# Kernel tuning notes

Hardware: AMD Instinct MI355X
Metric: run time of the kernel (lower is better)

Reference implementation:

```python
import jax, jax.numpy as jnp
import numpy as np

H = 64
IN = 3
OUT = 4


def _lstm_layer(x, w_ih, w_hh, b_ih, b_hh):
    # x: [B, T, D_in]; w_ih: [4H, D_in]; w_hh: [4H, H]; PyTorch gate order i,f,g,o
    B = x.shape[0]
    gx = jnp.einsum('btd,gd->btg', x, w_ih) + b_ih + b_hh  # [B, T, 4H]
    gx_t = jnp.swapaxes(gx, 0, 1)  # [T, B, 4H]

    def step(carry, g_t):
        h, c = carry
        g = g_t + h @ w_hh.T
        i, f, gg, o = jnp.split(g, 4, axis=-1)
        i = jax.nn.sigmoid(i)
        f = jax.nn.sigmoid(f)
        gg = jnp.tanh(gg)
        o = jax.nn.sigmoid(o)
        c = f * c + i * gg
        h = o * jnp.tanh(c)
        return (h, c), h

    init = (jnp.zeros((B, H), x.dtype), jnp.zeros((B, H), x.dtype))
    _, hs = jax.lax.scan(step, init, gx_t)
    return jnp.swapaxes(hs, 0, 1)  # [B, T, H]


def setup_inputs() -> dict:
    key = jax.random.key(0)
    ks = jax.random.split(key, 12)
    s = 1.0 / np.sqrt(H)

    def u(k, shape):
        return jax.random.uniform(k, shape, jnp.float32, -s, s)

    x = jax.random.normal(ks[0], (1024, 512, IN), jnp.float32)
    return {
        'x': x,
        'w_ih0': u(ks[1], (4 * H, IN)),
        'w_hh0': u(ks[2], (4 * H, H)),
        'b_ih0': u(ks[3], (4 * H,)),
        'b_hh0': u(ks[4], (4 * H,)),
        'w_ih1': u(ks[5], (4 * H, H)),
        'w_hh1': u(ks[6], (4 * H, H)),
        'b_ih1': u(ks[7], (4 * H,)),
        'b_hh1': u(ks[8], (4 * H,)),
        'w_out': u(ks[9], (OUT, H)),
        'b_out': u(ks[10], (OUT,)),
    }


def reference(x, w_ih0, w_hh0, b_ih0, b_hh0, w_ih1, w_hh1, b_ih1, b_hh1, w_out, b_out):
    h1 = _lstm_layer(x, w_ih0, w_hh0, b_ih0, b_hh0)   # [B, T, H]
    h2 = _lstm_layer(h1, w_ih1, w_hh1, b_ih1, b_hh1)  # [B, T, H]
    logits = h2[:, -1, :] @ w_out.T + b_out           # [B, OUT]
    return jax.nn.softmax(logits, axis=1)
```

## Files before the change

kernel.cpp:

```cpp
#include <hip/hip_runtime.h>

#define TT    512
#define HH    64
#define NB    4
#define NBLK  256
#define HP    80

#define LOG2E 1.44269504f

typedef _Float16 f16x8 __attribute__((ext_vector_type(8)));
typedef float    f32x4 __attribute__((ext_vector_type(4)));

#if __has_builtin(__builtin_amdgcn_exp2f)
#define EXP2(x) __builtin_amdgcn_exp2f(x)
#else
#define EXP2(x) exp2f(x)
#endif

__device__ __forceinline__ float sig2_(float xs) {
    return __builtin_amdgcn_rcpf(1.0f + EXP2(xs));
}
__device__ __forceinline__ float tanh2_(float xs) {
    return 1.0f - 2.0f * __builtin_amdgcn_rcpf(1.0f + EXP2(xs));
}

__global__ __launch_bounds__(512) void lstm_mfma(
    const float* __restrict__ x,
    const float* __restrict__ w_ih0, const float* __restrict__ w_hh0,
    const float* __restrict__ b_ih0, const float* __restrict__ b_hh0,
    const float* __restrict__ w_ih1, const float* __restrict__ w_hh1,
    const float* __restrict__ b_ih1, const float* __restrict__ b_hh1,
    const float* __restrict__ w_out, const float* __restrict__ b_out,
    float* __restrict__ out)
{
    __shared__ __align__(16) _Float16 h1T[2][4 * HP];
    __shared__ __align__(16) _Float16 h2T[2][4 * HP];
    __shared__ float xs[TT * 12];
    __shared__ __align__(16) float h2f[4 * 68];
    __shared__ float lg[NB][4];

    const int tid   = threadIdx.x;
    const int group = tid >> 8;
    const int w     = (tid >> 6) & 3;
    const int lane  = tid & 63;
    const int quad  = lane >> 4;
    const int n     = lane & 15;
    const int bq    = n >> 2;
    const int b0    = blockIdx.x * NB;

    f16x8 whh[4][2], wih[4][2], axf[4];
    f32x4 biasf[4];
    #pragma unroll
    for (int g_ = 0; g_ < 4; ++g_) {
        const float sc = (g_ == 2) ? (2.0f * LOG2E) : (-LOG2E);
        const int arow = 16 * w + 64 * g_ + n;
        const float* ph = (group == 0) ? (w_hh0 + arow * HH) : (w_hh1 + arow * HH);
        const float* pi = w_ih1 + arow * HH;
        #pragma unroll
        for (int k0 = 0; k0 < 2; ++k0) {
            #pragma unroll
            for (int j = 0; j < 8; ++j) {
                whh[g_][k0][j] = (_Float16)(sc * ph[quad * 8 + 32 * k0 + j]);
                wih[g_][k0][j] = (group == 1) ? (_Float16)(sc * pi[quad * 8 + 32 * k0 + j])
                                              : (_Float16)0.f;
            }
        }
        const float bv = sc * ((group == 0) ? (b_ih0[arow] + b_hh0[arow])
                                            : (b_ih1[arow] + b_hh1[arow]));
        #pragma unroll
        for (int r = 0; r < 4; ++r) biasf[g_][r] = bv;
        f16x8 ax;
        #pragma unroll
        for (int j = 0; j < 8; ++j) ax[j] = (_Float16)0.f;
        if (group == 0 && quad == 0) {
            ax[0] = (_Float16)(sc * w_ih0[arow * 3 + 0]);
            ax[1] = (_Float16)(sc * w_ih0[arow * 3 + 1]);
            ax[2] = (_Float16)(sc * w_ih0[arow * 3 + 2]);
        }
        axf[g_] = ax;
    }

    for (int i = tid; i < 2 * 4 * HP / 2; i += 512) {
        ((int*)h1T)[i] = 0;
        ((int*)h2T)[i] = 0;
    }
    for (int i = tid; i < TT * 12; i += 512) {
        const int t = i / 12, rem = i - t * 12;
        const int d = rem >> 2, b = rem & 3;
        xs[i] = x[(size_t)(b0 + b) * (TT * 3) + t * 3 + d];
    }
    __syncthreads();

    float creg = 0.f;

    for (int t = 0; t <= TT; ++t) {
        if (group == 0) {
            if (t < TT) {
                f16x8 bx;
                #pragma unroll
                for (int j = 0; j < 8; ++j) bx[j] = (_Float16)0.f;
                if (quad == 0) {
                    const float* xp = xs + t * 12 + bq;
                    bx[0] = (_Float16)xp[0];
                    bx[1] = (_Float16)xp[4];
                    bx[2] = (_Float16)xp[8];
                }
                const _Float16* hsrc = h1T[(t + 1) & 1];
                const f16x8 bh0 = *(const f16x8*)(hsrc + bq * HP + quad * 8);
                const f16x8 bh1 = *(const f16x8*)(hsrc + bq * HP + quad * 8 + 32);
                f32x4 acc[4];
                #pragma unroll
                for (int g_ = 0; g_ < 4; ++g_) {
                    f32x4 a = __builtin_amdgcn_mfma_f32_16x16x32_f16(bx, axf[g_], biasf[g_], 0, 0, 0);
                    a = __builtin_amdgcn_mfma_f32_16x16x32_f16(bh0, whh[g_][0], a, 0, 0, 0);
                    a = __builtin_amdgcn_mfma_f32_16x16x32_f16(bh1, whh[g_][1], a, 0, 0, 0);
                    acc[g_] = a;
                }
                const float is = sig2_(acc[0][0]);
                const float fs = sig2_(acc[1][0]);
                const float gt = tanh2_(acc[2][0]);
                const float os = sig2_(acc[3][0]);
                creg = fs * creg + is * gt;
                h1T[t & 1][quad * HP + 16 * w + n] =
                    (_Float16)(os * tanh2_(creg * (2.0f * LOG2E)));
            }
        } else {
            if (t >= 1) {
                const _Float16* h1src = h1T[(t + 1) & 1];
                const _Float16* h2src = h2T[(t + 1) & 1];
                const f16x8 b10 = *(const f16x8*)(h1src + bq * HP + quad * 8);
                const f16x8 b11 = *(const f16x8*)(h1src + bq * HP + quad * 8 + 32);
                const f16x8 b20 = *(const f16x8*)(h2src + bq * HP + quad * 8);
                const f16x8 b21 = *(const f16x8*)(h2src + bq * HP + quad * 8 + 32);
                f32x4 acc[4];
                #pragma unroll
                for (int g_ = 0; g_ < 4; ++g_) {
                    f32x4 a = __builtin_amdgcn_mfma_f32_16x16x32_f16(b10, wih[g_][0], biasf[g_], 0, 0, 0);
                    a = __builtin_amdgcn_mfma_f32_16x16x32_f16(b11, wih[g_][1], a, 0, 0, 0);
                    a = __builtin_amdgcn_mfma_f32_16x16x32_f16(b20, whh[g_][0], a, 0, 0, 0);
                    a = __builtin_amdgcn_mfma_f32_16x16x32_f16(b21, whh[g_][1], a, 0, 0, 0);
                    acc[g_] = a;
                }
                const float is = sig2_(acc[0][0]);
                const float fs = sig2_(acc[1][0]);
                const float gt = tanh2_(acc[2][0]);
                const float os = sig2_(acc[3][0]);
                creg = fs * creg + is * gt;
                const float h = os * tanh2_(creg * (2.0f * LOG2E));
                h2T[t & 1][quad * HP + 16 * w + n] = (_Float16)h;
                if (t == TT) h2f[quad * 68 + 16 * w + n] = h;
            }
        }
        __syncthreads();
    }

    if (tid < 16) {
        const int b = tid & 3, o = tid >> 2;
        float acc = b_out[o];
        #pragma unroll
        for (int j = 0; j < HH; ++j)
            acc = fmaf(w_out[o * HH + j], h2f[b * 68 + j], acc);
        lg[b][o] = acc;
    }
    __syncthreads();
    if (tid < NB) {
        const int b = tid;
        const float l0 = lg[b][0], l1 = lg[b][1], l2 = lg[b][2], l3 = lg[b][3];
        const float m  = fmaxf(fmaxf(l0, l1), fmaxf(l2, l3));
        const float e0 = __expf(l0 - m), e1 = __expf(l1 - m);
        const float e2 = __expf(l2 - m), e3 = __expf(l3 - m);
        const float sum = 1.0f / (e0 + e1 + e2 + e3);
        out[(b0 + b) * 4 + 0] = e0 * sum;
        out[(b0 + b) * 4 + 1] = e1 * sum;
        out[(b0 + b) * 4 + 2] = e2 * sum;
        out[(b0 + b) * 4 + 3] = e3 * sum;
    }
}

extern "C" void kernel_launch(void* const* d_in, const int* in_sizes, int n_in,
                              void* d_out, int out_size, void* d_ws, size_t ws_size,
                              hipStream_t stream) {
    const float* x     = (const float*)d_in[0];
    const float* w_ih0 = (const float*)d_in[1];
    const float* w_hh0 = (const float*)d_in[2];
    const float* b_ih0 = (const float*)d_in[3];
    const float* b_hh0 = (const float*)d_in[4];
    const float* w_ih1 = (const float*)d_in[5];
    const float* w_hh1 = (const float*)d_in[6];
    const float* b_ih1 = (const float*)d_in[7];
    const float* b_hh1 = (const float*)d_in[8];
    const float* w_out = (const float*)d_in[9];
    const float* b_out = (const float*)d_in[10];
    float* out = (float*)d_out;

    hipLaunchKernelGGL(lstm_mfma, dim3(NBLK), dim3(512), 0, stream,
                       x, w_ih0, w_hh0, b_ih0, b_hh0,
                       w_ih1, w_hh1, b_ih1, b_hh1,
                       w_out, b_out, out);
}
```

Measured before the change: 301.7 us.

## Halve block size so each wave computes two hidden-unit tiles per step

Blocks shrink from 512 to 256 threads, with two waves per LSTM layer instead of four. Each wave now holds twice the weight fragments and computes two 16-unit hidden tiles per timestep, keeping two cell states in registers. The aim is cheaper per-step block barriers and more MFMA work per wave between syncs. The cost is doubled register pressure for weights and a longer serial MFMA chain per wave on the recurrent critical path.

```diff
diff --git a/kernel.cpp b/kernel.cpp
--- a/kernel.cpp
+++ b/kernel.cpp
@@ -24,7 +24,7 @@
     return 1.0f - 2.0f * __builtin_amdgcn_rcpf(1.0f + EXP2(xs));
 }
 
-__global__ __launch_bounds__(512) void lstm_mfma(
+__global__ __launch_bounds__(256, 1) void lstm_mfma(
     const float* __restrict__ x,
     const float* __restrict__ w_ih0, const float* __restrict__ w_hh0,
     const float* __restrict__ b_ih0, const float* __restrict__ b_hh0,
@@ -40,35 +40,35 @@
     __shared__ float lg[NB][4];
 
     const int tid   = threadIdx.x;
-    const int group = tid >> 8;
-    const int w     = (tid >> 6) & 3;
+    const int group = tid >> 7;
+    const int w     = (tid >> 6) & 1;
     const int lane  = tid & 63;
     const int quad  = lane >> 4;
     const int n     = lane & 15;
     const int bq    = n >> 2;
     const int b0    = blockIdx.x * NB;
 
-    f16x8 whh[4][2], wih[4][2], axf[4];
-    f32x4 biasf[4];
+    f16x8 whh[8][2], wih[8][2], axf[8];
+    f32x4 biasf[8];
     #pragma unroll
-    for (int g_ = 0; g_ < 4; ++g_) {
-        const float sc = (g_ == 2) ? (2.0f * LOG2E) : (-LOG2E);
-        const int arow = 16 * w + 64 * g_ + n;
+    for (int g8 = 0; g8 < 8; ++g8) {
+        const float sc = ((g8 >> 1) == 2) ? (2.0f * LOG2E) : (-LOG2E);
+        const int arow = 16 * w + 32 * g8 + n;
         const float* ph = (group == 0) ? (w_hh0 + arow * HH) : (w_hh1 + arow * HH);
         const float* pi = w_ih1 + arow * HH;
         #pragma unroll
         for (int k0 = 0; k0 < 2; ++k0) {
             #pragma unroll
             for (int j = 0; j < 8; ++j) {
-                whh[g_][k0][j] = (_Float16)(sc * ph[quad * 8 + 32 * k0 + j]);
-                wih[g_][k0][j] = (group == 1) ? (_Float16)(sc * pi[quad * 8 + 32 * k0 + j])
+                whh[g8][k0][j] = (_Float16)(sc * ph[quad * 8 + 32 * k0 + j]);
+                wih[g8][k0][j] = (group == 1) ? (_Float16)(sc * pi[quad * 8 + 32 * k0 + j])
                                               : (_Float16)0.f;
             }
         }
         const float bv = sc * ((group == 0) ? (b_ih0[arow] + b_hh0[arow])
                                             : (b_ih1[arow] + b_hh1[arow]));
         #pragma unroll
-        for (int r = 0; r < 4; ++r) biasf[g_][r] = bv;
+        for (int r = 0; r < 4; ++r) biasf[g8][r] = bv;
         f16x8 ax;
         #pragma unroll
         for (int j = 0; j < 8; ++j) ax[j] = (_Float16)0.f;
@@ -77,21 +77,21 @@
             ax[1] = (_Float16)(sc * w_ih0[arow * 3 + 1]);
             ax[2] = (_Float16)(sc * w_ih0[arow * 3 + 2]);
         }
-        axf[g_] = ax;
-    }
-
-    for (int i = tid; i < 2 * 4 * HP / 2; i += 512) {
+        axf[g8] = ax;
+    }
+
+    for (int i = tid; i < 2 * 4 * HP / 2; i += 256) {
         ((int*)h1T)[i] = 0;
         ((int*)h2T)[i] = 0;
     }
-    for (int i = tid; i < TT * 12; i += 512) {
+    for (int i = tid; i < TT * 12; i += 256) {
         const int t = i / 12, rem = i - t * 12;
         const int d = rem >> 2, b = rem & 3;
         xs[i] = x[(size_t)(b0 + b) * (TT * 3) + t * 3 + d];
     }
     __syncthreads();
 
-    float creg = 0.f;
+    float creg[2] = {0.f, 0.f};
 
     for (int t = 0; t <= TT; ++t) {
         if (group == 0) {
@@ -108,21 +108,24 @@
                 const _Float16* hsrc = h1T[(t + 1) & 1];
                 const f16x8 bh0 = *(const f16x8*)(hsrc + bq * HP + quad * 8);
                 const f16x8 bh1 = *(const f16x8*)(hsrc + bq * HP + quad * 8 + 32);
-                f32x4 acc[4];
-                #pragma unroll
-                for (int g_ = 0; g_ < 4; ++g_) {
-                    f32x4 a = __builtin_amdgcn_mfma_f32_16x16x32_f16(bx, axf[g_], biasf[g_], 0, 0, 0);
-                    a = __builtin_amdgcn_mfma_f32_16x16x32_f16(bh0, whh[g_][0], a, 0, 0, 0);
-                    a = __builtin_amdgcn_mfma_f32_16x16x32_f16(bh1, whh[g_][1], a, 0, 0, 0);
-                    acc[g_] = a;
-                }
-                const float is = sig2_(acc[0][0]);
-                const float fs = sig2_(acc[1][0]);
-                const float gt = tanh2_(acc[2][0]);
-                const float os = sig2_(acc[3][0]);
-                creg = fs * creg + is * gt;
-                h1T[t & 1][quad * HP + 16 * w + n] =
-                    (_Float16)(os * tanh2_(creg * (2.0f * LOG2E)));
+                f32x4 acc[8];
+                #pragma unroll
+                for (int g8 = 0; g8 < 8; ++g8) {
+                    f32x4 a = __builtin_amdgcn_mfma_f32_16x16x32_f16(bx, axf[g8], biasf[g8], 0, 0, 0);
+                    a = __builtin_amdgcn_mfma_f32_16x16x32_f16(bh0, whh[g8][0], a, 0, 0, 0);
+                    a = __builtin_amdgcn_mfma_f32_16x16x32_f16(bh1, whh[g8][1], a, 0, 0, 0);
+                    acc[g8] = a;
+                }
+                #pragma unroll
+                for (int h = 0; h < 2; ++h) {
+                    const float is = sig2_(acc[0 + h][0]);
+                    const float fs = sig2_(acc[2 + h][0]);
+                    const float gt = tanh2_(acc[4 + h][0]);
+                    const float os = sig2_(acc[6 + h][0]);
+                    creg[h] = fs * creg[h] + is * gt;
+                    h1T[t & 1][quad * HP + 32 * h + 16 * w + n] =
+                        (_Float16)(os * tanh2_(creg[h] * (2.0f * LOG2E)));
+                }
             }
         } else {
             if (t >= 1) {
@@ -132,23 +135,26 @@
                 const f16x8 b11 = *(const f16x8*)(h1src + bq * HP + quad * 8 + 32);
                 const f16x8 b20 = *(const f16x8*)(h2src + bq * HP + quad * 8);
                 const f16x8 b21 = *(const f16x8*)(h2src + bq * HP + quad * 8 + 32);
-                f32x4 acc[4];
-                #pragma unroll
-                for (int g_ = 0; g_ < 4; ++g_) {
-                    f32x4 a = __builtin_amdgcn_mfma_f32_16x16x32_f16(b10, wih[g_][0], biasf[g_], 0, 0, 0);
-                    a = __builtin_amdgcn_mfma_f32_16x16x32_f16(b11, wih[g_][1], a, 0, 0, 0);
-                    a = __builtin_amdgcn_mfma_f32_16x16x32_f16(b20, whh[g_][0], a, 0, 0, 0);
-                    a = __builtin_amdgcn_mfma_f32_16x16x32_f16(b21, whh[g_][1], a, 0, 0, 0);
-                    acc[g_] = a;
-                }
-                const float is = sig2_(acc[0][0]);
-                const float fs = sig2_(acc[1][0]);
-                const float gt = tanh2_(acc[2][0]);
-                const float os = sig2_(acc[3][0]);
-                creg = fs * creg + is * gt;
-                const float h = os * tanh2_(creg * (2.0f * LOG2E));
-                h2T[t & 1][quad * HP + 16 * w + n] = (_Float16)h;
-                if (t == TT) h2f[quad * 68 + 16 * w + n] = h;
+                f32x4 acc[8];
+                #pragma unroll
+                for (int g8 = 0; g8 < 8; ++g8) {
+                    f32x4 a = __builtin_amdgcn_mfma_f32_16x16x32_f16(b10, wih[g8][0], biasf[g8], 0, 0, 0);
+                    a = __builtin_amdgcn_mfma_f32_16x16x32_f16(b11, wih[g8][1], a, 0, 0, 0);
+                    a = __builtin_amdgcn_mfma_f32_16x16x32_f16(b20, whh[g8][0], a, 0, 0, 0);
+                    a = __builtin_amdgcn_mfma_f32_16x16x32_f16(b21, whh[g8][1], a, 0, 0, 0);
+                    acc[g8] = a;
+                }
+                #pragma unroll
+                for (int h = 0; h < 2; ++h) {
+                    const float is = sig2_(acc[0 + h][0]);
+                    const float fs = sig2_(acc[2 + h][0]);
+                    const float gt = tanh2_(acc[4 + h][0]);
+                    const float os = sig2_(acc[6 + h][0]);
+                    creg[h] = fs * creg[h] + is * gt;
+                    const float hh_ = os * tanh2_(creg[h] * (2.0f * LOG2E));
+                    h2T[t & 1][quad * HP + 32 * h + 16 * w + n] = (_Float16)hh_;
+                    if (t == TT) h2f[quad * 68 + 32 * h + 16 * w + n] = hh_;
+                }
             }
         }
         __syncthreads();
@@ -193,7 +199,7 @@
     const float* b_out = (const float*)d_in[10];
     float* out = (float*)d_out;
 
-    hipLaunchKernelGGL(lstm_mfma, dim3(NBLK), dim3(512), 0, stream,
+    hipLaunchKernelGGL(lstm_mfma, dim3(NBLK), dim3(256), 0, stream,
                        x, w_ih0, w_hh0, b_ih0, b_hh0,
                        w_ih1, w_hh1, b_ih1, b_hh1,
                        w_out, b_out, out);
```

After: 386.4 us. 1.28x slower.
